# Performance work log

Hardware: AMD Instinct MI355X
Metric: run time of the kernel (lower is better)

Reference implementation:

```python
import jax, jax.numpy as jnp
import numpy as np

N_NODES = 50000
N_EDGES = 800000
IN_DIM = 256
HID = 64          # per-head hidden dim
HEADS = 4
OUT_DIM = 64
NEG_SLOPE = 0.2


def setup_inputs() -> dict:
    key = jax.random.key(0)
    ks = jax.random.split(key, 10)
    x = jax.random.normal(ks[0], (N_NODES, IN_DIM), dtype=jnp.float32)
    src = jax.random.randint(ks[1], (N_EDGES,), 0, N_NODES, dtype=jnp.int32)
    dst = jax.random.randint(ks[2], (N_EDGES,), 0, N_NODES, dtype=jnp.int32)
    # layer 1: IN_DIM -> HEADS x HID (concat)
    W1 = jax.random.normal(ks[3], (IN_DIM, HEADS * HID), dtype=jnp.float32) * (1.0 / np.sqrt(IN_DIM))
    al1 = jax.random.normal(ks[4], (HEADS, HID), dtype=jnp.float32) * 0.1
    ar1 = jax.random.normal(ks[5], (HEADS, HID), dtype=jnp.float32) * 0.1
    W2 = jax.random.normal(ks[6], (HEADS * HID, 1 * OUT_DIM), dtype=jnp.float32) * (1.0 / np.sqrt(HEADS * HID))
    al2 = jax.random.normal(ks[7], (1, OUT_DIM), dtype=jnp.float32) * 0.1
    ar2 = jax.random.normal(ks[8], (1, OUT_DIM), dtype=jnp.float32) * 0.1
    return {"x": x, "src": src, "dst": dst, "W1": W1, "al1": al1, "ar1": ar1,
            "W2": W2, "al2": al2, "ar2": ar2}


def gat_layer(h, src, dst, W, al, ar):
    # h: [N, F_in]; W: [F_in, H*D]; al/ar: [H, D]
    H, D = al.shape
    feat = (h @ W).reshape(-1, H, D)                       # [N, H, D]
    el = jnp.einsum('nhd,hd->nh', feat, al)                # [N, H]
    er = jnp.einsum('nhd,hd->nh', feat, ar)                # [N, H]
    e = jax.nn.leaky_relu(el[src] + er[dst], negative_slope=NEG_SLOPE)  # [E, H]
    # softmax over incoming edges of each destination node
    m = jax.ops.segment_max(e, dst, num_segments=N_NODES)  # [N, H]
    w = jnp.exp(e - m[dst])                                # [E, H]
    s = jax.ops.segment_sum(w, dst, num_segments=N_NODES)  # [N, H]
    alpha = w / s[dst]                                     # [E, H]
    msg = feat[src] * alpha[:, :, None]                    # [E, H, D]
    out = jax.ops.segment_sum(msg, dst, num_segments=N_NODES)  # [N, H, D]
    return out


def reference(x, src, dst, W1, al1, ar1, W2, al2, ar2):
    # layer 1: concat heads + elu (dropout disabled: eval mode)
    h1 = gat_layer(x, src, dst, W1, al1, ar1)              # [N, HEADS, HID]
    h1 = jax.nn.elu(h1.reshape(N_NODES, HEADS * HID))      # [N, HEADS*HID]
    # output layer: single head, mean over heads (trivial for H=1)
    h2 = gat_layer(h1, src, dst, W2, al2, ar2)             # [N, 1, OUT_DIM]
    logits = h2.mean(axis=1)                               # [N, OUT_DIM]
    return logits
```

## Files before the change

### kernel.cpp

```cpp
#include <hip/hip_runtime.h>
#include <math.h>

#define NNODES 50000
#define NEDGES 800000
#define INDIM 256
#define HID 64
#define HEADS 4
#define OUTDIM 64
#define NEG_SLOPE 0.2f
#define NB ((NNODES + 1023) / 1024)

typedef __attribute__((ext_vector_type(4))) float f32x4;
typedef _Float16 __attribute__((ext_vector_type(8))) half8;


__global__ __launch_bounds__(256) void hist_kernel(const int* __restrict__ dst,
                                                   int* __restrict__ deg) {
    int i = blockIdx.x * 256 + threadIdx.x;
    if (i < NEDGES) atomicAdd(&deg[dst[i]], 1);
}

__global__ __launch_bounds__(256) void bsum_kernel(const int* __restrict__ deg,
                                                   int* __restrict__ bsums) {
    int b = blockIdx.x, t = threadIdx.x;
    int base = b * 1024 + t * 4;
    int s = 0;
    #pragma unroll
    for (int e = 0; e < 4; ++e) { int i = base + e; if (i < NNODES) s += deg[i]; }
    #pragma unroll
    for (int o = 32; o; o >>= 1) s += __shfl_xor(s, o);
    __shared__ int ws[4];
    int lane = t & 63, wid = t >> 6;
    if (lane == 0) ws[wid] = s;
    __syncthreads();
    if (t == 0) bsums[b] = ws[0] + ws[1] + ws[2] + ws[3];
}

__global__ __launch_bounds__(256) void scan_write_kernel(const int* __restrict__ deg,
                                                         const int* __restrict__ bsums,
                                                         int* __restrict__ offs) {
    int b = blockIdx.x, t = threadIdx.x;
    int lane = t & 63, wid = t >> 6;
    int bv = (lane < b) ? bsums[lane] : 0;
    #pragma unroll
    for (int o = 32; o; o >>= 1) bv += __shfl_xor(bv, o);
    int base = b * 1024 + t * 4;
    int v[4]; int tsum = 0;
    #pragma unroll
    for (int e = 0; e < 4; ++e) {
        int i = base + e;
        v[e] = (i < NNODES) ? deg[i] : 0;
        tsum += v[e];
    }
    int p = tsum;
    #pragma unroll
    for (int o = 1; o < 64; o <<= 1) { int u = __shfl_up(p, o); if (lane >= o) p += u; }
    __shared__ int ws[4];
    if (lane == 63) ws[wid] = p;
    __syncthreads();
    int woff = 0;
    for (int i = 0; i < wid; ++i) woff += ws[i];
    int run = bv + woff + p - tsum;
    #pragma unroll
    for (int e = 0; e < 4; ++e) {
        int i = base + e;
        if (i < NNODES) { offs[i] = run; run += v[e]; }
    }
    if (b == 0 && t == 0) offs[NNODES] = NEDGES;
}

__global__ __launch_bounds__(256) void scatter_kernel(const int* __restrict__ src,
                                                      const int* __restrict__ dst,
                                                      const int* __restrict__ offs,
                                                      int* __restrict__ cursor,
                                                      int* __restrict__ ssorted) {
    int i = blockIdx.x * 256 + threadIdx.x;
    if (i < NEDGES) {
        int d = dst[i];
        int pos = offs[d] + atomicAdd(&cursor[d], 1);
        ssorted[pos] = src[i];
    }
}


__global__ __launch_bounds__(256) void convert_wt_kernel(const float* __restrict__ W1,
                                                         _Float16* __restrict__ W1t,
                                                         const float* __restrict__ W2,
                                                         _Float16* __restrict__ W2t) {
    int idx = blockIdx.x * 256 + threadIdx.x;
    if (idx < 256 * 256) {
        int k = idx >> 8, n = idx & 255;
        W1t[n * 256 + k] = (_Float16)W1[idx];
    } else if (idx < 256 * 256 + 256 * 64) {
        int j = idx - 256 * 256;
        int k = j >> 6, n = j & 63;
        W2t[n * 256 + k] = (_Float16)W2[j];
    }
}


__global__ __launch_bounds__(256) void convert_x_kernel(const float* __restrict__ x,
                                                        _Float16* __restrict__ xh) {
    int i = blockIdx.x * 256 + threadIdx.x;
    if (i < NNODES * (INDIM / 8)) {
        const float4* xp = (const float4*)x;
        float4 f0 = xp[(size_t)i * 2];
        float4 f1 = xp[(size_t)i * 2 + 1];
        half8 v;
        v[0] = (_Float16)f0.x; v[1] = (_Float16)f0.y;
        v[2] = (_Float16)f0.z; v[3] = (_Float16)f0.w;
        v[4] = (_Float16)f1.x; v[5] = (_Float16)f1.y;
        v[6] = (_Float16)f1.z; v[7] = (_Float16)f1.w;
        ((half8*)xh)[i] = v;
    }
}


template <int BM, int BN, bool AFP16, int ELR>
__global__ __launch_bounds__(256) void gemm_f16_kernel(
        const float* __restrict__ Af, const _Float16* __restrict__ Ah,
        const _Float16* __restrict__ Bt,
        _Float16* __restrict__ C,
        const float* __restrict__ al, const float* __restrict__ ar,
        float* __restrict__ el, float* __restrict__ er,
        int M, int N) {
    constexpr int K = 256;
    constexpr int NT = BN / 32;
    constexpr int TM = BM / 32;
    int t = threadIdx.x;
    int lane = t & 63, w = t >> 6;
    int wm = w >> 1, wn = w & 1;
    int lr = lane & 15, quad = lane >> 4;
    int m0 = blockIdx.y * BM, n0 = blockIdx.x * BN;

    f32x4 acc[TM][NT];
    #pragma unroll
    for (int i = 0; i < TM; ++i)
        #pragma unroll
        for (int j = 0; j < NT; ++j) acc[i][j] = (f32x4){0.f, 0.f, 0.f, 0.f};

    int arow[TM];
    #pragma unroll
    for (int i = 0; i < TM; ++i) {
        int r = m0 + wm * (BM / 2) + i * 16 + lr;
        arow[i] = (r < M) ? r : (M - 1);
    }
    int brow[NT];
    #pragma unroll
    for (int j = 0; j < NT; ++j) brow[j] = n0 + wn * NT * 16 + j * 16 + lr;

    #pragma unroll
    for (int kk = 0; kk < K; kk += 32) {
        half8 a[TM], b[NT];
        if (AFP16) {
            #pragma unroll
            for (int i = 0; i < TM; ++i)
                a[i] = *(const half8*)(Ah + (size_t)arow[i] * K + kk + quad * 8);
        } else {
            #pragma unroll
            for (int i = 0; i < TM; ++i) {
                const float* ap = Af + (size_t)arow[i] * K + kk + quad * 8;
                float4 f0 = *(const float4*)ap;
                float4 f1 = *(const float4*)(ap + 4);
                a[i][0] = (_Float16)f0.x; a[i][1] = (_Float16)f0.y;
                a[i][2] = (_Float16)f0.z; a[i][3] = (_Float16)f0.w;
                a[i][4] = (_Float16)f1.x; a[i][5] = (_Float16)f1.y;
                a[i][6] = (_Float16)f1.z; a[i][7] = (_Float16)f1.w;
            }
        }
        #pragma unroll
        for (int j = 0; j < NT; ++j)
            b[j] = *(const half8*)(Bt + (size_t)brow[j] * K + kk + quad * 8);
        #pragma unroll
        for (int i = 0; i < TM; ++i)
            #pragma unroll
            for (int j = 0; j < NT; ++j)
                acc[i][j] = __builtin_amdgcn_mfma_f32_16x16x32_f16(a[i], b[j], acc[i][j], 0, 0, 0);
    }
    #pragma unroll
    for (int i = 0; i < TM; ++i) {
        #pragma unroll
        for (int r = 0; r < 4; ++r) {
            int row = m0 + wm * (BM / 2) + i * 16 + quad * 4 + r;
            if (row < M) {
                #pragma unroll
                for (int j = 0; j < NT; ++j)
                    C[(size_t)row * N + n0 + wn * NT * 16 + j * 16 + lr] =
                        (_Float16)acc[i][j][r];
            }
        }
    }
    if constexpr (ELR == 1) {
        int h = n0 / 64 + wn;
        float alh[NT], arh[NT];
        #pragma unroll
        for (int j = 0; j < NT; ++j) {
            alh[j] = al[h * 64 + j * 16 + lr];
            arh[j] = ar[h * 64 + j * 16 + lr];
        }
        #pragma unroll
        for (int i = 0; i < TM; ++i) {
            #pragma unroll
            for (int r = 0; r < 4; ++r) {
                float pel = 0.f, per = 0.f;
                #pragma unroll
                for (int j = 0; j < NT; ++j) {
                    pel = fmaf(acc[i][j][r], alh[j], pel);
                    per = fmaf(acc[i][j][r], arh[j], per);
                }
                #pragma unroll
                for (int o = 1; o < 16; o <<= 1) {
                    pel += __shfl_xor(pel, o);
                    per += __shfl_xor(per, o);
                }
                if (lr == 0) {
                    int row = m0 + wm * (BM / 2) + i * 16 + quad * 4 + r;
                    if (row < M) {
                        el[(size_t)row * 4 + h] = pel;
                        er[(size_t)row * 4 + h] = per;
                    }
                }
            }
        }
    }
    if constexpr (ELR == 2) {
        __shared__ float elbuf[BM], erbuf[BM];
        float alv[NT], arv[NT];
        #pragma unroll
        for (int j = 0; j < NT; ++j) {
            alv[j] = al[wn * NT * 16 + j * 16 + lr];
            arv[j] = ar[wn * NT * 16 + j * 16 + lr];
        }
        float pel_s[TM][4], per_s[TM][4];
        #pragma unroll
        for (int i = 0; i < TM; ++i) {
            #pragma unroll
            for (int r = 0; r < 4; ++r) {
                float pel = 0.f, per = 0.f;
                #pragma unroll
                for (int j = 0; j < NT; ++j) {
                    pel = fmaf(acc[i][j][r], alv[j], pel);
                    per = fmaf(acc[i][j][r], arv[j], per);
                }
                #pragma unroll
                for (int o = 1; o < 16; o <<= 1) {
                    pel += __shfl_xor(pel, o);
                    per += __shfl_xor(per, o);
                }
                pel_s[i][r] = pel; per_s[i][r] = per;
            }
        }
        if (wn == 1 && lr == 0) {
            #pragma unroll
            for (int i = 0; i < TM; ++i)
                #pragma unroll
                for (int r = 0; r < 4; ++r) {
                    int rl = wm * (BM / 2) + i * 16 + quad * 4 + r;
                    elbuf[rl] = pel_s[i][r];
                    erbuf[rl] = per_s[i][r];
                }
        }
        __syncthreads();
        if (wn == 0 && lr == 0) {
            #pragma unroll
            for (int i = 0; i < TM; ++i)
                #pragma unroll
                for (int r = 0; r < 4; ++r) {
                    int rl = wm * (BM / 2) + i * 16 + quad * 4 + r;
                    int row = m0 + rl;
                    if (row < M) {
                        el[row] = pel_s[i][r] + elbuf[rl];
                        er[row] = per_s[i][r] + erbuf[rl];
                    }
                }
        }
    }
}


__global__ __launch_bounds__(256) void spmm1_kernel(const _Float16* __restrict__ feat,
                                                    const float* __restrict__ el,
                                                    const float* __restrict__ er,
                                                    const int* __restrict__ offs,
                                                    const int* __restrict__ ssorted,
                                                    _Float16* __restrict__ h1) {
    int n = blockIdx.x * 4 + (threadIdx.x >> 6);
    if (n >= NNODES) return;
    int l = threadIdx.x & 63;
    int p2 = l >> 5;
    int q  = l & 31;
    int h  = q >> 3;
    int start = offs[n], end = offs[n + 1];
    int nst = (end - start + 1) >> 1;
    float ern = er[(size_t)n * 4 + h];
    const half8* f8 = (const half8*)feat;
    float acc[8];
    #pragma unroll
    for (int i = 0; i < 8; ++i) acc[i] = 0.f;
    float ws = 0.f;
    half8 z;
    #pragma unroll
    for (int i = 0; i < 8; ++i) z[i] = (_Float16)0;
    int sjB = 0, sjN = 0;
    float elA = 0.f, elB = 0.f;
    half8 fvA = z, fvB = z;
    if (nst > 0) {
        int x0 = start + p2;
        int sjA = ssorted[x0 < end ? x0 : start];
        if (nst > 1) {
            int x1 = start + 2 + p2;
            sjB = ssorted[x1 < end ? x1 : start];
        }
        elA = el[(size_t)sjA * 4 + h];
        fvA = f8[(size_t)sjA * 32 + q];
    }
    for (int js = 0; js < nst; ++js) {
        if (js + 1 < nst) {
            elB = el[(size_t)sjB * 4 + h];
            fvB = f8[(size_t)sjB * 32 + q];
        }
        if (js + 2 < nst) {
            int x = start + (js + 2) * 2 + p2;
            sjN = ssorted[x < end ? x : start];
        }
        bool vld = (start + js * 2 + p2) < end;
        float ev = elA + ern;
        ev = ev > 0.f ? ev : NEG_SLOPE * ev;
        float w = vld ? __expf(ev) : 0.f;
        ws += w;
        #pragma unroll
        for (int i = 0; i < 8; ++i) acc[i] = fmaf(w, (float)fvA[i], acc[i]);
        elA = elB; fvA = fvB; sjB = sjN;
    }
    ws += __shfl_xor(ws, 32);
    #pragma unroll
    for (int i = 0; i < 8; ++i) acc[i] += __shfl_xor(acc[i], 32);
    if (l < 32) {
        float inv = ws > 0.f ? 1.f / ws : 0.f;
        half8 hv;
        #pragma unroll
        for (int i = 0; i < 8; ++i) {
            float v = acc[i] * inv;
            v = v > 0.f ? v : __expf(v) - 1.f;
            hv[i] = (_Float16)v;
        }
        *(half8*)&h1[(size_t)n * 256 + q * 8] = hv;
    }
}


__global__ __launch_bounds__(256) void spmm2_kernel(const _Float16* __restrict__ feat,
                                                    const float* __restrict__ el,
                                                    const float* __restrict__ er,
                                                    const int* __restrict__ offs,
                                                    const int* __restrict__ ssorted,
                                                    float* __restrict__ out) {
    int n = blockIdx.x * 4 + (threadIdx.x >> 6);
    if (n >= NNODES) return;
    int l = threadIdx.x & 63;
    int e8 = l >> 3, li = l & 7;
    int start = offs[n], end = offs[n + 1];
    int nst = (end - start + 7) >> 3;
    float ern = er[n];
    const half8* f8 = (const half8*)feat;
    float acc[8];
    #pragma unroll
    for (int i = 0; i < 8; ++i) acc[i] = 0.f;
    float ws = 0.f;
    half8 z;
    #pragma unroll
    for (int i = 0; i < 8; ++i) z[i] = (_Float16)0;
    int sjB = 0, sjN = 0;
    float elA = 0.f, elB = 0.f;
    half8 fvA = z, fvB = z;
    if (nst > 0) {
        int x0 = start + e8;
        int sjA = ssorted[x0 < end ? x0 : start];
        if (nst > 1) {
            int x1 = start + 8 + e8;
            sjB = ssorted[x1 < end ? x1 : start];
        }
        elA = el[sjA];
        fvA = f8[(size_t)sjA * 8 + li];
    }
    for (int js = 0; js < nst; ++js) {
        if (js + 1 < nst) {
            elB = el[sjB];
            fvB = f8[(size_t)sjB * 8 + li];
        }
        if (js + 2 < nst) {
            int x = start + (js + 2) * 8 + e8;
            sjN = ssorted[x < end ? x : start];
        }
        bool vld = (start + js * 8 + e8) < end;
        float ev = elA + ern;
        ev = ev > 0.f ? ev : NEG_SLOPE * ev;
        float w = vld ? __expf(ev) : 0.f;
        ws += w;
        #pragma unroll
        for (int i = 0; i < 8; ++i) acc[i] = fmaf(w, (float)fvA[i], acc[i]);
        elA = elB; fvA = fvB; sjB = sjN;
    }
    #pragma unroll
    for (int o = 8; o < 64; o <<= 1) {
        ws += __shfl_xor(ws, o);
        #pragma unroll
        for (int i = 0; i < 8; ++i) acc[i] += __shfl_xor(acc[i], o);
    }
    if (e8 == 0) {
        float inv = ws > 0.f ? 1.f / ws : 0.f;
        float4 o0, o1;
        o0.x = acc[0] * inv; o0.y = acc[1] * inv;
        o0.z = acc[2] * inv; o0.w = acc[3] * inv;
        o1.x = acc[4] * inv; o1.y = acc[5] * inv;
        o1.z = acc[6] * inv; o1.w = acc[7] * inv;
        float4* op = (float4*)(out + (size_t)n * 64 + li * 8);
        op[0] = o0; op[1] = o1;
    }
}


extern "C" void kernel_launch(void* const* d_in, const int* in_sizes, int n_in,
                              void* d_out, int out_size, void* d_ws, size_t ws_size,
                              hipStream_t stream) {
    const float* x   = (const float*)d_in[0];
    const int*   src = (const int*)d_in[1];
    const int*   dst = (const int*)d_in[2];
    const float* W1  = (const float*)d_in[3];
    const float* al1 = (const float*)d_in[4];
    const float* ar1 = (const float*)d_in[5];
    const float* W2  = (const float*)d_in[6];
    const float* al2 = (const float*)d_in[7];
    const float* ar2 = (const float*)d_in[8];
    float* out = (float*)d_out;

    char* ws = (char*)d_ws;
    size_t off = 0;
    auto alloc = [&](size_t bytes) -> void* {
        void* p = ws + off;
        off += (bytes + 255) & ~(size_t)255;
        return p;
    };
    _Float16* feat1 = (_Float16*)alloc((size_t)NNODES * 256 * 2);
    _Float16* h1    = (_Float16*)alloc((size_t)NNODES * 256 * 2);
    _Float16* W1t   = (_Float16*)alloc((size_t)256 * 256 * 2);
    _Float16* W2t   = (_Float16*)alloc((size_t)64 * 256 * 2);
    float* el1    = (float*)alloc((size_t)NNODES * 4 * 4);
    float* er1    = (float*)alloc((size_t)NNODES * 4 * 4);
    float* el2    = (float*)alloc((size_t)NNODES * 4);
    float* er2    = (float*)alloc((size_t)NNODES * 4);
    int* deg      = (int*)alloc((size_t)NNODES * 4);
    int* cursor   = (int*)alloc((size_t)NNODES * 4);
    int* offs     = (int*)alloc((size_t)(NNODES + 1) * 4);
    int* bsums    = (int*)alloc((size_t)NB * 4);
    int* ssorted  = (int*)alloc((size_t)NEDGES * 4);
    _Float16* feat2 = feat1;
    _Float16* xh = h1;

    hipMemsetAsync(deg, 0, (size_t)NNODES * 4, stream);
    hipMemsetAsync(cursor, 0, (size_t)NNODES * 4, stream);
    hist_kernel<<<(NEDGES + 255) / 256, 256, 0, stream>>>(dst, deg);
    bsum_kernel<<<NB, 256, 0, stream>>>(deg, bsums);
    scan_write_kernel<<<NB, 256, 0, stream>>>(deg, bsums, offs);
    scatter_kernel<<<(NEDGES + 255) / 256, 256, 0, stream>>>(src, dst, offs, cursor, ssorted);

    convert_wt_kernel<<<(256 * 256 + 256 * 64 + 255) / 256, 256, 0, stream>>>(
        W1, W1t, W2, W2t);
    convert_x_kernel<<<(NNODES * (INDIM / 8) + 255) / 256, 256, 0, stream>>>(x, xh);

    gemm_f16_kernel<64, 128, true, 1><<<dim3(256 / 128, (NNODES + 63) / 64), 256, 0, stream>>>(
        nullptr, xh, W1t, feat1, al1, ar1, el1, er1, NNODES, 256);
    spmm1_kernel<<<(NNODES + 3) / 4, 256, 0, stream>>>(
        feat1, el1, er1, offs, ssorted, h1);

    gemm_f16_kernel<64, 64, true, 2><<<dim3(64 / 64, (NNODES + 63) / 64), 256, 0, stream>>>(
        nullptr, h1, W2t, feat2, al2, ar2, el2, er2, NNODES, 64);
    spmm2_kernel<<<(NNODES + 3) / 4, 256, 0, stream>>>(
        feat2, el2, er2, offs, ssorted, out);
}
```

Before: 338.4 us.

## Merge independent prep kernels and overlap GEMM1 with the CSR scatter

The histogram, x-to-fp16 conversion and weight transpose-conversion now run as branches of one prep launch keyed on block index. The CSR scatter now runs as extra blocks of the first GEMM launch, so the scatter overlaps the matmul. This cuts the number of kernel launches and fills idle compute units during short phases. The merged kernels use more registers under a single launch configuration, which may lower occupancy for the light branches.

```diff
diff --git a/kernel.cpp b/kernel.cpp
--- a/kernel.cpp
+++ b/kernel.cpp
@@ -9,16 +9,13 @@
 #define OUTDIM 64
 #define NEG_SLOPE 0.2f
 #define NB ((NNODES + 1023) / 1024)
+#define HB ((NEDGES + 255) / 256)
+#define XB ((NNODES * (INDIM / 8) + 255) / 256)
+#define WB ((256 * 256 + 256 * 64 + 255) / 256)
 
 typedef __attribute__((ext_vector_type(4))) float f32x4;
 typedef _Float16 __attribute__((ext_vector_type(8))) half8;
 
-
-__global__ __launch_bounds__(256) void hist_kernel(const int* __restrict__ dst,
-                                                   int* __restrict__ deg) {
-    int i = blockIdx.x * 256 + threadIdx.x;
-    if (i < NEDGES) atomicAdd(&deg[dst[i]], 1);
-}
 
 __global__ __launch_bounds__(256) void bsum_kernel(const int* __restrict__ deg,
                                                    int* __restrict__ bsums) {
@@ -69,61 +66,54 @@
     if (b == 0 && t == 0) offs[NNODES] = NEDGES;
 }
 
-__global__ __launch_bounds__(256) void scatter_kernel(const int* __restrict__ src,
-                                                      const int* __restrict__ dst,
-                                                      const int* __restrict__ offs,
-                                                      int* __restrict__ cursor,
-                                                      int* __restrict__ ssorted) {
-    int i = blockIdx.x * 256 + threadIdx.x;
-    if (i < NEDGES) {
-        int d = dst[i];
-        int pos = offs[d] + atomicAdd(&cursor[d], 1);
-        ssorted[pos] = src[i];
-    }
-}
-
-
-__global__ __launch_bounds__(256) void convert_wt_kernel(const float* __restrict__ W1,
-                                                         _Float16* __restrict__ W1t,
-                                                         const float* __restrict__ W2,
-                                                         _Float16* __restrict__ W2t) {
-    int idx = blockIdx.x * 256 + threadIdx.x;
-    if (idx < 256 * 256) {
-        int k = idx >> 8, n = idx & 255;
-        W1t[n * 256 + k] = (_Float16)W1[idx];
-    } else if (idx < 256 * 256 + 256 * 64) {
-        int j = idx - 256 * 256;
-        int k = j >> 6, n = j & 63;
-        W2t[n * 256 + k] = (_Float16)W2[j];
-    }
-}
-
-
-__global__ __launch_bounds__(256) void convert_x_kernel(const float* __restrict__ x,
-                                                        _Float16* __restrict__ xh) {
-    int i = blockIdx.x * 256 + threadIdx.x;
-    if (i < NNODES * (INDIM / 8)) {
-        const float4* xp = (const float4*)x;
-        float4 f0 = xp[(size_t)i * 2];
-        float4 f1 = xp[(size_t)i * 2 + 1];
-        half8 v;
-        v[0] = (_Float16)f0.x; v[1] = (_Float16)f0.y;
-        v[2] = (_Float16)f0.z; v[3] = (_Float16)f0.w;
-        v[4] = (_Float16)f1.x; v[5] = (_Float16)f1.y;
-        v[6] = (_Float16)f1.z; v[7] = (_Float16)f1.w;
-        ((half8*)xh)[i] = v;
-    }
-}
-
-
-template <int BM, int BN, bool AFP16, int ELR>
-__global__ __launch_bounds__(256) void gemm_f16_kernel(
-        const float* __restrict__ Af, const _Float16* __restrict__ Ah,
+
+__global__ __launch_bounds__(256) void prep_kernel(const int* __restrict__ dst,
+                                                   int* __restrict__ deg,
+                                                   const float* __restrict__ W1,
+                                                   _Float16* __restrict__ W1t,
+                                                   const float* __restrict__ W2,
+                                                   _Float16* __restrict__ W2t,
+                                                   const float* __restrict__ x,
+                                                   _Float16* __restrict__ xh) {
+    int b = blockIdx.x;
+    if (b < HB) {
+        int i = b * 256 + threadIdx.x;
+        if (i < NEDGES) atomicAdd(&deg[dst[i]], 1);
+    } else if (b < HB + XB) {
+        int i = (b - HB) * 256 + threadIdx.x;
+        if (i < NNODES * (INDIM / 8)) {
+            const float4* xp = (const float4*)x;
+            float4 f0 = xp[(size_t)i * 2];
+            float4 f1 = xp[(size_t)i * 2 + 1];
+            half8 v;
+            v[0] = (_Float16)f0.x; v[1] = (_Float16)f0.y;
+            v[2] = (_Float16)f0.z; v[3] = (_Float16)f0.w;
+            v[4] = (_Float16)f1.x; v[5] = (_Float16)f1.y;
+            v[6] = (_Float16)f1.z; v[7] = (_Float16)f1.w;
+            ((half8*)xh)[i] = v;
+        }
+    } else {
+        int idx = (b - HB - XB) * 256 + threadIdx.x;
+        if (idx < 256 * 256) {
+            int k = idx >> 8, n = idx & 255;
+            W1t[n * 256 + k] = (_Float16)W1[idx];
+        } else if (idx < 256 * 256 + 256 * 64) {
+            int j = idx - 256 * 256;
+            int k = j >> 6, n = j & 63;
+            W2t[n * 256 + k] = (_Float16)W2[j];
+        }
+    }
+}
+
+
+template <int BM, int BN, int ELR>
+__device__ __forceinline__ void gemm_body(
+        const _Float16* __restrict__ Ah,
         const _Float16* __restrict__ Bt,
         _Float16* __restrict__ C,
         const float* __restrict__ al, const float* __restrict__ ar,
         float* __restrict__ el, float* __restrict__ er,
-        int M, int N) {
+        int M, int N, int m0, int n0) {
     constexpr int K = 256;
     constexpr int NT = BN / 32;
     constexpr int TM = BM / 32;
@@ -131,7 +121,6 @@
     int lane = t & 63, w = t >> 6;
     int wm = w >> 1, wn = w & 1;
     int lr = lane & 15, quad = lane >> 4;
-    int m0 = blockIdx.y * BM, n0 = blockIdx.x * BN;
 
     f32x4 acc[TM][NT];
     #pragma unroll
@@ -152,22 +141,9 @@
     #pragma unroll
     for (int kk = 0; kk < K; kk += 32) {
         half8 a[TM], b[NT];
-        if (AFP16) {
-            #pragma unroll
-            for (int i = 0; i < TM; ++i)
-                a[i] = *(const half8*)(Ah + (size_t)arow[i] * K + kk + quad * 8);
-        } else {
-            #pragma unroll
-            for (int i = 0; i < TM; ++i) {
-                const float* ap = Af + (size_t)arow[i] * K + kk + quad * 8;
-                float4 f0 = *(const float4*)ap;
-                float4 f1 = *(const float4*)(ap + 4);
-                a[i][0] = (_Float16)f0.x; a[i][1] = (_Float16)f0.y;
-                a[i][2] = (_Float16)f0.z; a[i][3] = (_Float16)f0.w;
-                a[i][4] = (_Float16)f1.x; a[i][5] = (_Float16)f1.y;
-                a[i][6] = (_Float16)f1.z; a[i][7] = (_Float16)f1.w;
-            }
-        }
+        #pragma unroll
+        for (int i = 0; i < TM; ++i)
+            a[i] = *(const half8*)(Ah + (size_t)arow[i] * K + kk + quad * 8);
         #pragma unroll
         for (int j = 0; j < NT; ++j)
             b[j] = *(const half8*)(Bt + (size_t)brow[j] * K + kk + quad * 8);
@@ -275,6 +251,42 @@
                 }
         }
     }
+}
+
+
+__global__ __launch_bounds__(256) void gemm1_scatter_kernel(
+        const _Float16* __restrict__ Ah, const _Float16* __restrict__ Bt,
+        _Float16* __restrict__ C,
+        const float* __restrict__ al, const float* __restrict__ ar,
+        float* __restrict__ el, float* __restrict__ er,
+        int gemmBlocks,
+        const int* __restrict__ src, const int* __restrict__ dst,
+        const int* __restrict__ offs, int* __restrict__ cursor,
+        int* __restrict__ ssorted) {
+    int b = blockIdx.x;
+    if (b < gemmBlocks) {
+        int m0 = (b >> 1) * 64, n0 = (b & 1) * 128;
+        gemm_body<64, 128, 1>(Ah, Bt, C, al, ar, el, er, NNODES, 256, m0, n0);
+    } else {
+        int i = (b - gemmBlocks) * 256 + threadIdx.x;
+        if (i < NEDGES) {
+            int d = dst[i];
+            int pos = offs[d] + atomicAdd(&cursor[d], 1);
+            ssorted[pos] = src[i];
+        }
+    }
+}
+
+
+template <int BM, int BN, int ELR>
+__global__ __launch_bounds__(256) void gemm_f16_kernel(
+        const _Float16* __restrict__ Ah, const _Float16* __restrict__ Bt,
+        _Float16* __restrict__ C,
+        const float* __restrict__ al, const float* __restrict__ ar,
+        float* __restrict__ el, float* __restrict__ er,
+        int M, int N) {
+    int m0 = blockIdx.y * BM, n0 = blockIdx.x * BN;
+    gemm_body<BM, BN, ELR>(Ah, Bt, C, al, ar, el, er, M, N, m0, n0);
 }
 
 
@@ -459,22 +471,22 @@
 
     hipMemsetAsync(deg, 0, (size_t)NNODES * 4, stream);
     hipMemsetAsync(cursor, 0, (size_t)NNODES * 4, stream);
-    hist_kernel<<<(NEDGES + 255) / 256, 256, 0, stream>>>(dst, deg);
+
+    prep_kernel<<<HB + XB + WB, 256, 0, stream>>>(dst, deg, W1, W1t, W2, W2t, x, xh);
+
     bsum_kernel<<<NB, 256, 0, stream>>>(deg, bsums);
     scan_write_kernel<<<NB, 256, 0, stream>>>(deg, bsums, offs);
-    scatter_kernel<<<(NEDGES + 255) / 256, 256, 0, stream>>>(src, dst, offs, cursor, ssorted);
-
-    convert_wt_kernel<<<(256 * 256 + 256 * 64 + 255) / 256, 256, 0, stream>>>(
-        W1, W1t, W2, W2t);
-    convert_x_kernel<<<(NNODES * (INDIM / 8) + 255) / 256, 256, 0, stream>>>(x, xh);
-
-    gemm_f16_kernel<64, 128, true, 1><<<dim3(256 / 128, (NNODES + 63) / 64), 256, 0, stream>>>(
-        nullptr, xh, W1t, feat1, al1, ar1, el1, er1, NNODES, 256);
+
+    int gemmBlocks = ((NNODES + 63) / 64) * 2;
+    gemm1_scatter_kernel<<<gemmBlocks + HB, 256, 0, stream>>>(
+        xh, W1t, feat1, al1, ar1, el1, er1, gemmBlocks,
+        src, dst, offs, cursor, ssorted);
+
     spmm1_kernel<<<(NNODES + 3) / 4, 256, 0, stream>>>(
         feat1, el1, er1, offs, ssorted, h1);
 
-    gemm_f16_kernel<64, 64, true, 2><<<dim3(64 / 64, (NNODES + 63) / 64), 256, 0, stream>>>(
-        nullptr, h1, W2t, feat2, al2, ar2, el2, er2, NNODES, 64);
+    gemm_f16_kernel<64, 64, 2><<<dim3(1, (NNODES + 63) / 64), 256, 0, stream>>>(
+        h1, W2t, feat2, al2, ar2, el2, er2, NNODES, 64);
     spmm2_kernel<<<(NNODES + 3) / 4, 256, 0, stream>>>(
         feat2, el2, er2, offs, ssorted, out);
 }
```

Measured after the change: 316.5 us. -6.5%, faster.
